# Kernel optimization log

Measured on AMD Instinct MI355X. Metric: run time of the kernel, lower is better.

Reference implementation:

```python
import jax, jax.numpy as jnp
import numpy as np

B, S, H, P = 8, 2048, 256, 64
NQ = 20

def setup_inputs() -> dict:
    key = jax.random.key(0)
    ks = jax.random.split(key, 12)
    s = lambda fan_in: 1.0 / np.sqrt(fan_in)
    return {
        "feature_x": jax.random.normal(ks[0], (B, S, H), dtype=jnp.float32),
        "param_x": jax.random.normal(ks[1], (B, S, P), dtype=jnp.float32),
        "sim_w1": jax.random.uniform(ks[2], (H, H // 2), jnp.float32, -s(H), s(H)),
        "sim_b1": jax.random.uniform(ks[3], (H // 2,), jnp.float32, -s(H), s(H)),
        "sim_w2": jax.random.uniform(ks[4], (H // 2, 1), jnp.float32, -s(H // 2), s(H // 2)),
        "sim_b2": jax.random.uniform(ks[5], (1,), jnp.float32, -s(H // 2), s(H // 2)),
        "conf_w1": jax.random.uniform(ks[6], (H, H // 2), jnp.float32, -s(H), s(H)),
        "conf_b1": jax.random.uniform(ks[7], (H // 2,), jnp.float32, -s(H), s(H)),
        "conf_w2": jax.random.uniform(ks[8], (H // 2, 1), jnp.float32, -s(H // 2), s(H // 2)),
        "conf_b2": jax.random.uniform(ks[9], (1,), jnp.float32, -s(H // 2), s(H // 2)),
        "questions": jax.random.randint(ks[10], (B, S), 0, NQ, dtype=jnp.int64 if jax.config.jax_enable_x64 else jnp.int32),
    }

def _mlp_scalar(x, w1, b1, w2, b2):
    # [B,S,H] -> [B,S] (dropout is eval-mode identity)
    h = jax.nn.relu(jnp.einsum("bsh,hk->bsk", x, w1) + b1)
    return (jnp.einsum("bsk,ko->bso", h, w2) + b2)[..., 0]

def reference(feature_x, param_x, sim_w1, sim_b1, sim_w2, sim_b2,
              conf_w1, conf_b1, conf_w2, conf_b2, questions):
    similarities = _mlp_scalar(feature_x, sim_w1, sim_b1, sim_w2, sim_b2)          # [B,S]
    confidences = jax.nn.sigmoid(_mlp_scalar(feature_x, conf_w1, conf_b1, conf_w2, conf_b2))  # [B,S]
    # multiplicative equality mask (zeros, not -inf, outside group — faithful to source)
    qmask = (questions[:, :, None] == questions[:, None, :]).astype(feature_x.dtype)  # [B,S,S]
    logits = similarities[:, :, None] * qmask                                        # [B,i,j]
    attn = jax.nn.softmax(logits, axis=-2)                                           # softmax over i
    smoothed = jnp.einsum("bij,bip->bjp", attn, param_x)                              # attn^T @ param_x
    c = confidences[..., None]
    return c * param_x + (1.0 - c) * smoothed
```

## Files before the change

### kernel.cpp

```cpp
#include <hip/hip_runtime.h>
#include <math.h>

#define B_  8
#define S_  2048
#define H_  256
#define HK_ 128
#define P_  64
#define NQ_ 20
#define M_  (B_*S_)
#define ACC_STRIDE (41*64)

__launch_bounds__(256)
__global__ void mlp_kernel(const float* __restrict__ fx,
                           const float* __restrict__ sw1, const float* __restrict__ sb1,
                           const float* __restrict__ sw2, const float* __restrict__ sb2,
                           const float* __restrict__ cw1, const float* __restrict__ cb1,
                           const float* __restrict__ cw2, const float* __restrict__ cb2,
                           float* __restrict__ sim, float* __restrict__ conf)
{
    const int tid = threadIdx.x;
    const int tx = tid & 15;
    const int ty = tid >> 4;
    const int row0 = blockIdx.x * 64;
    const bool isSim = (blockIdx.y == 0);
    const float* w1 = isSim ? sw1 : cw1;
    const float* b1 = isSim ? sb1 : cb1;
    const float* w2 = isSim ? sw2 : cw2;
    const float  b2v = isSim ? sb2[0] : cb2[0];

    __shared__ float As[16][68];
    __shared__ float Bs[16][128];

    float acc[4][8];
    #pragma unroll
    for (int r = 0; r < 4; ++r)
        #pragma unroll
        for (int c = 0; c < 8; ++c) acc[r][c] = 0.f;

    const int arow = tid >> 2;
    const int akc  = tid & 3;
    const int bk   = tid >> 5;
    const int bc4  = (tid & 31) * 4;

    for (int kb = 0; kb < H_; kb += 16) {
        float4 av  = *(const float4*)(fx + (size_t)(row0 + arow) * H_ + kb + akc * 4);
        float4 bv0 = *(const float4*)(w1 + (size_t)(kb + bk) * HK_ + bc4);
        float4 bv1 = *(const float4*)(w1 + (size_t)(kb + 8 + bk) * HK_ + bc4);
        __syncthreads();
        As[akc*4+0][arow] = av.x;
        As[akc*4+1][arow] = av.y;
        As[akc*4+2][arow] = av.z;
        As[akc*4+3][arow] = av.w;
        *(float4*)&Bs[bk  ][bc4] = bv0;
        *(float4*)&Bs[bk+8][bc4] = bv1;
        __syncthreads();
        #pragma unroll
        for (int k = 0; k < 16; ++k) {
            float4 a4  = *(const float4*)&As[k][ty*4];
            float4 b40 = *(const float4*)&Bs[k][tx*8];
            float4 b41 = *(const float4*)&Bs[k][tx*8+4];
            float a[4]  = {a4.x, a4.y, a4.z, a4.w};
            float bb[8] = {b40.x,b40.y,b40.z,b40.w,b41.x,b41.y,b41.z,b41.w};
            #pragma unroll
            for (int r = 0; r < 4; ++r)
                #pragma unroll
                for (int c = 0; c < 8; ++c)
                    acc[r][c] = fmaf(a[r], bb[c], acc[r][c]);
        }
    }

    float partial[4] = {0.f, 0.f, 0.f, 0.f};
    #pragma unroll
    for (int c = 0; c < 8; ++c) {
        int col = tx*8 + c;
        float b1c = b1[col];
        float w2c = w2[col];
        #pragma unroll
        for (int r = 0; r < 4; ++r)
            partial[r] += fmaxf(acc[r][c] + b1c, 0.f) * w2c;
    }
    #pragma unroll
    for (int off = 8; off >= 1; off >>= 1)
        #pragma unroll
        for (int r = 0; r < 4; ++r)
            partial[r] += __shfl_down(partial[r], off, 16);

    if (tx == 0) {
        #pragma unroll
        for (int r = 0; r < 4; ++r) {
            int grow = row0 + ty*4 + r;
            float v = partial[r] + b2v;
            if (isSim) sim[grow] = v;
            else       conf[grow] = 1.0f / (1.0f + expf(-v));
        }
    }
}

__global__ void denom_kernel(const float* __restrict__ sim, const int* __restrict__ questions,
                             float* __restrict__ denom)
{
    const int b = blockIdx.x / NQ_, q = blockIdx.x % NQ_;
    const float* simb = sim + b * S_;
    const int*   qb   = questions + b * S_;
    const int tid = threadIdx.x;
    float w = 0.f; int cnt = 0;
    for (int i = tid; i < S_; i += 256) {
        if (qb[i] == q) { w += expf(simb[i]); cnt++; }
    }
    #pragma unroll
    for (int off = 32; off >= 1; off >>= 1) {
        w   += __shfl_down(w, off, 64);
        cnt += __shfl_down(cnt, off, 64);
    }
    __shared__ float ws4[4];
    __shared__ int   cs4[4];
    if ((tid & 63) == 0) { ws4[tid >> 6] = w; cs4[tid >> 6] = cnt; }
    __syncthreads();
    if (tid == 0) {
        float W = ws4[0] + ws4[1] + ws4[2] + ws4[3];
        int   n = cs4[0] + cs4[1] + cs4[2] + cs4[3];
        denom[blockIdx.x] = (float)(S_ - n) + W;
    }
}

__launch_bounds__(256)
__global__ void accum_kernel(const float* __restrict__ sim, const int* __restrict__ questions,
                             const float* __restrict__ px, float* __restrict__ ws_acc)
{
    const int b = blockIdx.x;
    const int chunk = blockIdx.y;
    const int tid = threadIdx.x;
    const int lane = tid & 63;
    const int g = tid >> 6;
    __shared__ float accs[4][ACC_STRIDE];
    for (int s = tid; s < 4 * ACC_STRIDE; s += 256) ((float*)accs)[s] = 0.f;
    __syncthreads();

    const float* simb = sim + b * S_;
    const int*   qb   = questions + b * S_;
    const float* pxb  = px + (size_t)b * S_ * P_;

    float Treg = 0.f;
    const int i0 = chunk * 64 + g;
    for (int t = 0; t < 16; ++t) {
        int i = i0 + 4 * t;
        int qi = qb[i];
        float e = expf(simb[i]);
        float v = pxb[(size_t)i * P_ + lane];
        Treg += v;
        accs[g][qi * 64 + lane]        += v;
        accs[g][(20 + qi) * 64 + lane] += e * v;
    }
    accs[g][40 * 64 + lane] += Treg;
    __syncthreads();

    float* dst = ws_acc + (size_t)b * ACC_STRIDE;
    for (int s = tid; s < ACC_STRIDE; s += 256) {
        float sum = accs[0][s] + accs[1][s] + accs[2][s] + accs[3][s];
        atomicAdd(dst + s, sum);
    }
}

__global__ void output_kernel(const float* __restrict__ px, const float* __restrict__ conf,
                              const int* __restrict__ questions, const float* __restrict__ ws_acc,
                              const float* __restrict__ denom, float* __restrict__ out)
{
    const int idx = blockIdx.x * 256 + threadIdx.x;
    const int row = idx >> 4;
    const int p4  = idx & 15;
    const int b   = row >> 11;
    const float c = conf[row];
    const int   q = questions[row];
    const float* accb = ws_acc + (size_t)b * ACC_STRIDE;
    const float4 T = *(const float4*)(accb + 40 * 64 + p4 * 4);
    const float4 G = *(const float4*)(accb + q * 64 + p4 * 4);
    const float4 E = *(const float4*)(accb + (20 + q) * 64 + p4 * 4);
    const float inv = 1.0f / denom[b * NQ_ + q];
    const float4 pv = ((const float4*)px)[idx];
    const float om = 1.0f - c;
    float4 o;
    o.x = c * pv.x + om * ((T.x - G.x + E.x) * inv);
    o.y = c * pv.y + om * ((T.y - G.y + E.y) * inv);
    o.z = c * pv.z + om * ((T.z - G.z + E.z) * inv);
    o.w = c * pv.w + om * ((T.w - G.w + E.w) * inv);
    ((float4*)out)[idx] = o;
}

extern "C" void kernel_launch(void* const* d_in, const int* in_sizes, int n_in,
                              void* d_out, int out_size, void* d_ws, size_t ws_size,
                              hipStream_t stream) {
    const float* fx  = (const float*)d_in[0];
    const float* px  = (const float*)d_in[1];
    const float* sw1 = (const float*)d_in[2];
    const float* sb1 = (const float*)d_in[3];
    const float* sw2 = (const float*)d_in[4];
    const float* sb2 = (const float*)d_in[5];
    const float* cw1 = (const float*)d_in[6];
    const float* cb1 = (const float*)d_in[7];
    const float* cw2 = (const float*)d_in[8];
    const float* cb2 = (const float*)d_in[9];
    const int* questions = (const int*)d_in[10];
    float* out = (float*)d_out;

    float* ws     = (float*)d_ws;
    float* sim    = ws;
    float* conf   = ws + 16384;
    float* denom  = ws + 32768;
    float* ws_acc = ws + 33024;

    hipMemsetAsync(ws_acc, 0, (size_t)B_ * ACC_STRIDE * sizeof(float), stream);

    mlp_kernel<<<dim3(M_ / 64, 2), 256, 0, stream>>>(fx, sw1, sb1, sw2, sb2,
                                                     cw1, cb1, cw2, cb2, sim, conf);
    denom_kernel<<<B_ * NQ_, 256, 0, stream>>>(sim, questions, denom);
    accum_kernel<<<dim3(B_, 32), 256, 0, stream>>>(sim, questions, px, ws_acc);
    output_kernel<<<(M_ * P_ / 4) / 256, 256, 0, stream>>>(px, conf, questions,
                                                           ws_acc, denom, out);
}
```

Measured before the change: 128.3 us.

## Use bf16 MFMA with split-precision activations for MLP and fold denominators into accum

Replaces the scalar FP32 tiled MLP GEMM with a matrix-core kernel. A prep kernel converts both first-layer weight matrices to transposed bf16, and activations are split into hi and lo bf16 parts so two MFMAs approximate FP32 accuracy. The separate denom kernel and the memset are removed: per-question exp sums and counts are accumulated inside accum_kernel, and the prep kernel zeroes the accumulator buffer. Rounding the weights to bf16 loses some precision relative to FP32, and the weights are re-converted on every call.

```diff
diff --git a/kernel.cpp b/kernel.cpp
--- a/kernel.cpp
+++ b/kernel.cpp
@@ -8,118 +8,109 @@
 #define P_  64
 #define NQ_ 20
 #define M_  (B_*S_)
-#define ACC_STRIDE (41*64)
+#define ACC_STRIDE 2688
+
+#define WS_SIM   0
+#define WS_CONF  16384
+#define WS_ACC   32768
+#define WS_WT    54272
+
+typedef __attribute__((ext_vector_type(8))) short bf16x8;
+typedef __attribute__((ext_vector_type(4))) float f32x4;
+
+__global__ void prep_kernel(const float* __restrict__ sw1, const float* __restrict__ cw1,
+                            short* __restrict__ wt, float* __restrict__ ws_acc)
+{
+    const int t = blockIdx.x * 256 + threadIdx.x;
+    const int k = t & 255, n = (t >> 8) & 127, mlp = t >> 15;
+    const float* w1 = mlp ? cw1 : sw1;
+    union { float f; unsigned u; } c; c.f = w1[k * HK_ + n];
+    unsigned r = (c.u + 0x7FFF + ((c.u >> 16) & 1)) >> 16;
+    wt[t] = (short)r;
+    if (t < B_ * ACC_STRIDE) ws_acc[t] = 0.f;
+}
 
 __launch_bounds__(256)
-__global__ void mlp_kernel(const float* __restrict__ fx,
-                           const float* __restrict__ sw1, const float* __restrict__ sb1,
-                           const float* __restrict__ sw2, const float* __restrict__ sb2,
-                           const float* __restrict__ cw1, const float* __restrict__ cb1,
-                           const float* __restrict__ cw2, const float* __restrict__ cb2,
-                           float* __restrict__ sim, float* __restrict__ conf)
-{
-    const int tid = threadIdx.x;
-    const int tx = tid & 15;
-    const int ty = tid >> 4;
-    const int row0 = blockIdx.x * 64;
-    const bool isSim = (blockIdx.y == 0);
-    const float* w1 = isSim ? sw1 : cw1;
-    const float* b1 = isSim ? sb1 : cb1;
-    const float* w2 = isSim ? sw2 : cw2;
-    const float  b2v = isSim ? sb2[0] : cb2[0];
-
-    __shared__ float As[16][68];
-    __shared__ float Bs[16][128];
-
-    float acc[4][8];
+__global__ void mlp_mfma_kernel(const float* __restrict__ fx, const short* __restrict__ wt,
+                                const float* __restrict__ sb1, const float* __restrict__ sw2,
+                                const float* __restrict__ sb2, const float* __restrict__ cb1,
+                                const float* __restrict__ cw2, const float* __restrict__ cb2,
+                                float* __restrict__ sim, float* __restrict__ conf)
+{
+    __shared__ short lds[2 * 128 * 72];
+    const int tid  = threadIdx.x;
+    const int w    = tid >> 6, l = tid & 63;
+    const int col  = l & 15, quad = l >> 4;
+    const int mlp  = w >> 1, mt = w & 1;
+    const int row  = blockIdx.x * 32 + mt * 16 + col;
+
+    f32x4 acc[8];
     #pragma unroll
-    for (int r = 0; r < 4; ++r)
-        #pragma unroll
-        for (int c = 0; c < 8; ++c) acc[r][c] = 0.f;
-
-    const int arow = tid >> 2;
-    const int akc  = tid & 3;
-    const int bk   = tid >> 5;
-    const int bc4  = (tid & 31) * 4;
-
-    for (int kb = 0; kb < H_; kb += 16) {
-        float4 av  = *(const float4*)(fx + (size_t)(row0 + arow) * H_ + kb + akc * 4);
-        float4 bv0 = *(const float4*)(w1 + (size_t)(kb + bk) * HK_ + bc4);
-        float4 bv1 = *(const float4*)(w1 + (size_t)(kb + 8 + bk) * HK_ + bc4);
+    for (int nt = 0; nt < 8; ++nt) acc[nt] = (f32x4){0.f, 0.f, 0.f, 0.f};
+
+    const float* fxrow = fx + (size_t)row * H_;
+
+    for (int ch = 0; ch < 4; ++ch) {
         __syncthreads();
-        As[akc*4+0][arow] = av.x;
-        As[akc*4+1][arow] = av.y;
-        As[akc*4+2][arow] = av.z;
-        As[akc*4+3][arow] = av.w;
-        *(float4*)&Bs[bk  ][bc4] = bv0;
-        *(float4*)&Bs[bk+8][bc4] = bv1;
+        #pragma unroll
+        for (int i = 0; i < 8; ++i) {
+            int u  = tid + 256 * i;
+            int um = u >> 10, un = (u >> 3) & 127, us = u & 7;
+            const short* src = wt + um * 32768 + un * 256 + ch * 64 + us * 8;
+            *(uint4*)&lds[um * 9216 + un * 72 + us * 8] = *(const uint4*)src;
+        }
         __syncthreads();
         #pragma unroll
-        for (int k = 0; k < 16; ++k) {
-            float4 a4  = *(const float4*)&As[k][ty*4];
-            float4 b40 = *(const float4*)&Bs[k][tx*8];
-            float4 b41 = *(const float4*)&Bs[k][tx*8+4];
-            float a[4]  = {a4.x, a4.y, a4.z, a4.w};
-            float bb[8] = {b40.x,b40.y,b40.z,b40.w,b41.x,b41.y,b41.z,b41.w};
+        for (int ks = 0; ks < 2; ++ks) {
+            const int kg = ch * 64 + ks * 32 + quad * 8;
+            float4 a0 = *(const float4*)(fxrow + kg);
+            float4 a1 = *(const float4*)(fxrow + kg + 4);
+            float af[8] = {a0.x, a0.y, a0.z, a0.w, a1.x, a1.y, a1.z, a1.w};
+            bf16x8 ahi, alo;
             #pragma unroll
-            for (int r = 0; r < 4; ++r)
-                #pragma unroll
-                for (int c = 0; c < 8; ++c)
-                    acc[r][c] = fmaf(a[r], bb[c], acc[r][c]);
-        }
-    }
-
-    float partial[4] = {0.f, 0.f, 0.f, 0.f};
+            for (int i = 0; i < 8; ++i) {
+                union { float f; unsigned u; } c; c.f = af[i];
+                unsigned hi = c.u >> 16;
+                ahi[i] = (short)hi;
+                union { float f; unsigned u; } h2; h2.u = hi << 16;
+                union { float f; unsigned u; } c2; c2.f = af[i] - h2.f;
+                alo[i] = (short)(c2.u >> 16);
+            }
+            const short* bbase = lds + mlp * 9216 + ks * 32 + quad * 8;
+            #pragma unroll
+            for (int nt = 0; nt < 8; ++nt) {
+                bf16x8 bf = *(const bf16x8*)(bbase + (nt * 16 + col) * 72);
+                acc[nt] = __builtin_amdgcn_mfma_f32_16x16x32_bf16(ahi, bf, acc[nt], 0, 0, 0);
+                acc[nt] = __builtin_amdgcn_mfma_f32_16x16x32_bf16(alo, bf, acc[nt], 0, 0, 0);
+            }
+        }
+    }
+
+    const float* b1 = mlp ? cb1 : sb1;
+    const float* w2 = mlp ? cw2 : sw2;
+    const float  b2v = mlp ? cb2[0] : sb2[0];
+    float p[4] = {0.f, 0.f, 0.f, 0.f};
     #pragma unroll
-    for (int c = 0; c < 8; ++c) {
-        int col = tx*8 + c;
-        float b1c = b1[col];
-        float w2c = w2[col];
-        #pragma unroll
-        for (int r = 0; r < 4; ++r)
-            partial[r] += fmaxf(acc[r][c] + b1c, 0.f) * w2c;
+    for (int nt = 0; nt < 8; ++nt) {
+        float b1c = b1[nt * 16 + col];
+        float w2c = w2[nt * 16 + col];
+        #pragma unroll
+        for (int j = 0; j < 4; ++j)
+            p[j] += fmaxf(acc[nt][j] + b1c, 0.f) * w2c;
     }
     #pragma unroll
     for (int off = 8; off >= 1; off >>= 1)
         #pragma unroll
-        for (int r = 0; r < 4; ++r)
-            partial[r] += __shfl_down(partial[r], off, 16);
-
-    if (tx == 0) {
-        #pragma unroll
-        for (int r = 0; r < 4; ++r) {
-            int grow = row0 + ty*4 + r;
-            float v = partial[r] + b2v;
-            if (isSim) sim[grow] = v;
-            else       conf[grow] = 1.0f / (1.0f + expf(-v));
-        }
-    }
-}
-
-__global__ void denom_kernel(const float* __restrict__ sim, const int* __restrict__ questions,
-                             float* __restrict__ denom)
-{
-    const int b = blockIdx.x / NQ_, q = blockIdx.x % NQ_;
-    const float* simb = sim + b * S_;
-    const int*   qb   = questions + b * S_;
-    const int tid = threadIdx.x;
-    float w = 0.f; int cnt = 0;
-    for (int i = tid; i < S_; i += 256) {
-        if (qb[i] == q) { w += expf(simb[i]); cnt++; }
-    }
-    #pragma unroll
-    for (int off = 32; off >= 1; off >>= 1) {
-        w   += __shfl_down(w, off, 64);
-        cnt += __shfl_down(cnt, off, 64);
-    }
-    __shared__ float ws4[4];
-    __shared__ int   cs4[4];
-    if ((tid & 63) == 0) { ws4[tid >> 6] = w; cs4[tid >> 6] = cnt; }
-    __syncthreads();
-    if (tid == 0) {
-        float W = ws4[0] + ws4[1] + ws4[2] + ws4[3];
-        int   n = cs4[0] + cs4[1] + cs4[2] + cs4[3];
-        denom[blockIdx.x] = (float)(S_ - n) + W;
+        for (int j = 0; j < 4; ++j) p[j] += __shfl_down(p[j], off, 16);
+
+    if (col == 0) {
+        #pragma unroll
+        for (int j = 0; j < 4; ++j) {
+            int r = blockIdx.x * 32 + mt * 16 + quad * 4 + j;
+            float v = p[j] + b2v;
+            if (mlp == 0) sim[r] = v;
+            else          conf[r] = 1.0f / (1.0f + expf(-v));
+        }
     }
 }
 
@@ -150,8 +141,12 @@
         Treg += v;
         accs[g][qi * 64 + lane]        += v;
         accs[g][(20 + qi) * 64 + lane] += e * v;
-    }
-    accs[g][40 * 64 + lane] += Treg;
+        if (lane == 0) {
+            accs[g][2624 + qi] += e;
+            accs[g][2644 + qi] += 1.0f;
+        }
+    }
+    accs[g][2560 + lane] += Treg;
     __syncthreads();
 
     float* dst = ws_acc + (size_t)b * ACC_STRIDE;
@@ -163,7 +158,7 @@
 
 __global__ void output_kernel(const float* __restrict__ px, const float* __restrict__ conf,
                               const int* __restrict__ questions, const float* __restrict__ ws_acc,
-                              const float* __restrict__ denom, float* __restrict__ out)
+                              float* __restrict__ out)
 {
     const int idx = blockIdx.x * 256 + threadIdx.x;
     const int row = idx >> 4;
@@ -172,10 +167,11 @@
     const float c = conf[row];
     const int   q = questions[row];
     const float* accb = ws_acc + (size_t)b * ACC_STRIDE;
-    const float4 T = *(const float4*)(accb + 40 * 64 + p4 * 4);
+    const float4 T = *(const float4*)(accb + 2560 + p4 * 4);
     const float4 G = *(const float4*)(accb + q * 64 + p4 * 4);
     const float4 E = *(const float4*)(accb + (20 + q) * 64 + p4 * 4);
-    const float inv = 1.0f / denom[b * NQ_ + q];
+    const float denom = ((float)S_ - accb[2644 + q]) + accb[2624 + q];
+    const float inv = 1.0f / denom;
     const float4 pv = ((const float4*)px)[idx];
     const float om = 1.0f - c;
     float4 o;
@@ -203,17 +199,15 @@
     float* out = (float*)d_out;
 
     float* ws     = (float*)d_ws;
-    float* sim    = ws;
-    float* conf   = ws + 16384;
-    float* denom  = ws + 32768;
-    float* ws_acc = ws + 33024;
-
-    hipMemsetAsync(ws_acc, 0, (size_t)B_ * ACC_STRIDE * sizeof(float), stream);
-
-    mlp_kernel<<<dim3(M_ / 64, 2), 256, 0, stream>>>(fx, sw1, sb1, sw2, sb2,
-                                                     cw1, cb1, cw2, cb2, sim, conf);
-    denom_kernel<<<B_ * NQ_, 256, 0, stream>>>(sim, questions, denom);
+    float* sim    = ws + WS_SIM;
+    float* conf   = ws + WS_CONF;
+    float* ws_acc = ws + WS_ACC;
+    short* wt     = (short*)(ws + WS_WT);
+
+    prep_kernel<<<256, 256, 0, stream>>>(sw1, cw1, wt, ws_acc);
+    mlp_mfma_kernel<<<M_ / 32, 256, 0, stream>>>(fx, wt, sb1, sw2, sb2,
+                                                 cb1, cw2, cb2, sim, conf);
     accum_kernel<<<dim3(B_, 32), 256, 0, stream>>>(sim, questions, px, ws_acc);
     output_kernel<<<(M_ * P_ / 4) / 256, 256, 0, stream>>>(px, conf, questions,
-                                                           ws_acc, denom, out);
-}
+                                                           ws_acc, out);
+}
```

Result: faster. 117.7 us (-8.3%).
